# Kernel tuning notes

Hardware: AMD Instinct MI355X
Metric: run time of the kernel (lower is better)

## Reference

```python
import jax, jax.numpy as jnp
import numpy as np

B, N, D_FEAT = 4, 2048, 3
P = B * N
C_KP, K_PTS, NSAMPLE = 64, 15, 64
RADIUS, WINDOW = 0.2, 0.25
KP_EXTENT = 0.08  # prev_grid_size * sigma
F, H, HID, L = 256, 8, 512, 2
DH = F // H
EPS = 1e-5


def setup_inputs() -> dict:
    key = jax.random.key(0)
    k = jax.random.split(key, 24)
    s = 0.02
    position = jax.random.uniform(k[0], (B, N, 3), jnp.float32)
    feature = jax.random.normal(k[1], (B, N, D_FEAT), jnp.float32)
    # KPConv kernel points: fixed points inside a ball of radius 1.5*KP_EXTENT
    d = jax.random.normal(k[2], (K_PTS, 3))
    d = d / jnp.clip(jnp.linalg.norm(d, axis=1, keepdims=True), 1e-6)
    r = jax.random.uniform(k[3], (K_PTS, 1)) ** (1.0 / 3.0)
    kernel_points = (d * r * 1.5 * KP_EXTENT).astype(jnp.float32)
    return dict(
        position=position,
        feature=feature,
        kernel_points=kernel_points,
        kp_weights=s * jax.random.normal(k[4], (K_PTS, D_FEAT, C_KP), jnp.float32),
        bn_gamma=jnp.ones((C_KP,), jnp.float32),
        bn_beta=jnp.zeros((C_KP,), jnp.float32),
        weightmatrix=jax.random.normal(k[5], (1, C_KP + 3, F), jnp.float32) * s,
        Wq=s * jax.random.normal(k[6], (L, F, F), jnp.float32),
        bq=jnp.zeros((L, F), jnp.float32),
        Wk=s * jax.random.normal(k[7], (L, F, F), jnp.float32),
        bk=jnp.zeros((L, F), jnp.float32),
        Wv=s * jax.random.normal(k[8], (L, F, F), jnp.float32),
        bv=jnp.zeros((L, F), jnp.float32),
        Wo=s * jax.random.normal(k[9], (L, F, F), jnp.float32),
        bo=jnp.zeros((L, F), jnp.float32),
        ln1_g=jnp.ones((L, F), jnp.float32),
        ln1_b=jnp.zeros((L, F), jnp.float32),
        W1=s * jax.random.normal(k[10], (L, F, HID), jnp.float32),
        b1=jnp.zeros((L, HID), jnp.float32),
        W2=s * jax.random.normal(k[11], (L, HID, F), jnp.float32),
        b2=jnp.zeros((L, F), jnp.float32),
        ln2_g=jnp.ones((L, F), jnp.float32),
        ln2_b=jnp.zeros((L, F), jnp.float32),
    )


def _ball_query(position):
    """partial_dense ball query: first NSAMPLE in-radius neighbors per point, fill=P."""
    def one(b, pb):
        d2 = jnp.sum((pb[:, None, :] - pb[None, :, :]) ** 2, -1)      # [N,N]
        within = d2 <= RADIUS ** 2
        # stable argsort puts in-radius indices first, in ascending index order
        order = jnp.argsort(jnp.where(within, 0, 1).astype(jnp.int32), axis=1)[:, :NSAMPLE]
        valid = jnp.arange(NSAMPLE)[None, :] < jnp.sum(within, axis=1)[:, None]
        return jnp.where(valid, order + b * N, P)
    return jax.vmap(one)(jnp.arange(B), position).reshape(P, NSAMPLE)


def _kpconv(pos_flat, feat_flat, idx, kernel_points, kp_weights, bn_gamma, bn_beta):
    pos_pad = jnp.concatenate([pos_flat, jnp.full((1, 3), 1e6, pos_flat.dtype)], 0)
    feat_pad = jnp.concatenate([feat_flat, jnp.zeros((1, feat_flat.shape[1]), feat_flat.dtype)], 0)
    neigh = pos_pad[idx] - pos_flat[:, None, :]                     # [P,NS,3]
    diff = neigh[:, :, None, :] - kernel_points[None, None]         # [P,NS,K,3]
    dist = jnp.sqrt(jnp.sum(diff * diff, -1) + 1e-12)               # [P,NS,K]
    infl = jnp.clip(1.0 - dist / KP_EXTENT, 0.0)                    # linear influence
    nf = feat_pad[idx]                                              # [P,NS,Din]
    wf = jnp.einsum('pnk,pnd->pkd', infl, nf)
    out = jnp.einsum('pkd,kdc->pc', wf, kp_weights)                 # [P,C]
    mu = out.mean(0)
    var = out.var(0)
    out = bn_gamma * (out - mu) * jax.lax.rsqrt(var + EPS) + bn_beta
    return jnp.where(out >= 0, out, 0.2 * out)                      # LeakyReLU(0.2)


def _cluster_mask(position):
    """grid_sample: same-voxel points attend to each other. Returns bool [B,N,N]."""
    start = position.min(axis=1, keepdims=True)
    cell = jnp.floor((position - start) / WINDOW).astype(jnp.int32)
    cid = cell[..., 0] * 4096 + cell[..., 1] * 64 + cell[..., 2]
    return cid[:, :, None] == cid[:, None, :]


def _ln(x, g, b):
    mu = x.mean(-1, keepdims=True)
    v = x.var(-1, keepdims=True)
    return g * (x - mu) * jax.lax.rsqrt(v + EPS) + b


def _enc(x, mask, Wq, bq, Wk, bk, Wv, bv, Wo, bo, g1, be1, W1, bb1, W2, bb2, g2, be2):
    q = (x @ Wq + bq).reshape(B, N, H, DH)
    k = (x @ Wk + bk).reshape(B, N, H, DH)
    v = (x @ Wv + bv).reshape(B, N, H, DH)
    s = jnp.einsum('bihd,bjhd->bhij', q, k) * (1.0 / np.sqrt(DH))
    s = jnp.where(mask[:, None, :, :], s, -1e9)
    p = jax.nn.softmax(s, -1)
    o = jnp.einsum('bhij,bjhd->bihd', p, v).reshape(B, N, F)
    x = _ln(x + o @ Wo + bo, g1, be1)
    h = jax.nn.relu(x @ W1 + bb1) @ W2 + bb2
    return _ln(x + h, g2, be2)


def reference(position, feature, kernel_points, kp_weights, bn_gamma, bn_beta, weightmatrix,
              Wq, bq, Wk, bk, Wv, bv, Wo, bo, ln1_g, ln1_b, W1, b1, W2, b2, ln2_g, ln2_b):
    pos_flat = position.reshape(P, 3)
    feat_flat = feature.reshape(P, D_FEAT)
    idx = _ball_query(position)
    kpf = _kpconv(pos_flat, feat_flat, idx, kernel_points, kp_weights, bn_gamma, bn_beta)
    kpf = kpf.reshape(B, N, C_KP)
    mask = _cluster_mask(position)
    pw = jnp.concatenate([position, kpf], -1)                       # [B,N,C+3]
    emb = jnp.einsum('bnc,cf->bnf', pw, weightmatrix[0])
    for l in range(L):
        emb = _enc(emb, mask, Wq[l], bq[l], Wk[l], bk[l], Wv[l], bv[l], Wo[l], bo[l],
                   ln1_g[l], ln1_b[l], W1[l], b1[l], W2[l], b2[l], ln2_g[l], ln2_b[l])
    return emb
```

## Files before the change

kernel.cpp:

```cpp
#include <hip/hip_runtime.h>
#include <math.h>

#define BATCH 4
#define NPTS  2048
#define PTS   8192
#define NS    64
#define KPTS  15
#define CKP   64
#define FDIM  256
#define HIDD  512
#define NHEAD 8
#define DHEAD 32
#define NLAY  2
#define R2    0.04f
#define KPE   0.08f
#define WIN   0.25f
#define EPSF  1e-5f
#define SCALE 0.17677669529663687f
#define CPITCH 264

typedef __attribute__((ext_vector_type(8))) short          short8;
typedef __attribute__((ext_vector_type(8))) unsigned short ushort8;
typedef __attribute__((ext_vector_type(4))) float          f32x4;

static __device__ __forceinline__ unsigned short f2bf(float f) {
    unsigned int u = __float_as_uint(f);
    unsigned int r = u + 0x7fffu + ((u >> 16) & 1u);
    return (unsigned short)(r >> 16);
}
static __device__ __forceinline__ float b2f(unsigned short u) {
    return __uint_as_float(((unsigned int)u) << 16);
}

__global__ __launch_bounds__(256) void prep_k(
    const float* __restrict__ pos,
    const float* __restrict__ Wq, const float* __restrict__ Wk,
    const float* __restrict__ Wv, const float* __restrict__ Wo,
    const float* __restrict__ W1, const float* __restrict__ W2,
    const float* __restrict__ bq, const float* __restrict__ bk,
    const float* __restrict__ bv,
    unsigned short* __restrict__ wT, float* __restrict__ bqkv,
    int* __restrict__ sorted, int* __restrict__ inv,
    int* __restrict__ offs, int* __restrict__ hist,
    unsigned long long* __restrict__ masks)
{
    __shared__ __align__(16) unsigned char sm[38400];
    int bid = blockIdx.x, tid = threadIdx.x;

    if (bid < 3072) {
        int z = bid >> 8, r = bid & 255;
        int bx = r & 15, by = r >> 4;
        int t = z >> 1, l = z & 1;
        const float* src; unsigned short* dst; int K, N;
        switch (t) {
            case 0: src=Wq+(size_t)l*65536;  dst=wT+(size_t)l*196608;           K=256; N=256; break;
            case 1: src=Wk+(size_t)l*65536;  dst=wT+(size_t)l*196608+65536;     K=256; N=256; break;
            case 2: src=Wv+(size_t)l*65536;  dst=wT+(size_t)l*196608+131072;    K=256; N=256; break;
            case 3: src=Wo+(size_t)l*65536;  dst=wT+393216+(size_t)l*65536;     K=256; N=256; break;
            case 4: src=W1+(size_t)l*131072; dst=wT+524288+(size_t)l*131072;    K=256; N=512; break;
            default:src=W2+(size_t)l*131072; dst=wT+786432+(size_t)l*131072;    K=512; N=256; break;
        }
        int n0 = bx*32, k0 = by*32;
        if (n0 >= N || k0 >= K) return;
        float* ld = (float*)sm;
        #pragma unroll
        for (int i = 0; i < 4; ++i) { int v=tid+i*256; int ty=v>>5, tx=v&31;
            ld[ty*33+tx] = src[(size_t)(k0+ty)*N + n0+tx]; }
        __syncthreads();
        #pragma unroll
        for (int i = 0; i < 4; ++i) { int v=tid+i*256; int ny=v>>5, nk=v&31;
            dst[(size_t)(n0+ny)*K + k0+nk] = f2bf(ld[nk*33+ny]); }
    } else if (bid < 3584) {
        int m_ = bid - 3072;
        int chunk = m_ & 31, b = (m_ >> 5) & 3, qg = m_ >> 7;
        int w = tid >> 6, lane = tid & 63;
        float* qx = (float*)sm; float* qy = qx + 512; float* qz = qy + 512;
        int qbase = qg * 512;
        for (int t = tid; t < 512; t += 256) {
            const float* q = pos + (size_t)(b*NPTS + qbase + t)*3;
            qx[t] = q[0]; qy[t] = q[1]; qz[t] = q[2];
        }
        const float* c = pos + (size_t)(b*NPTS + chunk*64 + lane)*3;
        float cx = c[0], cy = c[1], cz = c[2];
        __syncthreads();
        int q0 = w * 128;
        for (int i = 0; i < 128; ++i) {
            int qi = q0 + i;
            float dx = cx - qx[qi], dy = cy - qy[qi], dz = cz - qz[qi];
            float d2 = dx*dx + dy*dy + dz*dz;
            unsigned long long m = __ballot(d2 <= R2);
            if (lane == 0) masks[(size_t)(b*NPTS + qbase + qi)*32 + chunk] = m;
        }
    } else if (bid < 3588) {
        int b = bid - 3584;
        float* sx = (float*)sm; float* sy = sx + 256; float* sz = sy + 256;
        unsigned char* cid_s = sm + 3072;
        unsigned int* maskc = (unsigned int*)(sm + 5120);
        int* wpfx = (int*)(sm + 21504);
        int* tot  = (int*)(sm + 37888);
        int* off_c= (int*)(sm + 38144);
        float mx=1e30f, my=1e30f, mz=1e30f;
        for (int n = tid; n < NPTS; n += 256) {
            const float* q = pos + ((size_t)b*NPTS + n)*3;
            mx = fminf(mx, q[0]); my = fminf(my, q[1]); mz = fminf(mz, q[2]);
        }
        sx[tid]=mx; sy[tid]=my; sz[tid]=mz; __syncthreads();
        for (int o=128;o;o>>=1){ if(tid<o){sx[tid]=fminf(sx[tid],sx[tid+o]);sy[tid]=fminf(sy[tid],sy[tid+o]);sz[tid]=fminf(sz[tid],sz[tid+o]);} __syncthreads(); }
        float X = sx[0], Y = sy[0], Z = sz[0];
        __syncthreads();
        for (int i = tid; i < 64*64; i += 256) maskc[i] = 0u;
        __syncthreads();
        for (int n = tid; n < NPTS; n += 256) {
            const float* q = pos + ((size_t)b*NPTS + n)*3;
            int cx = (int)floorf((q[0]-X)/WIN);
            int cy = (int)floorf((q[1]-Y)/WIN);
            int cz = (int)floorf((q[2]-Z)/WIN);
            int c = (cx<<4) | (cy<<2) | cz;
            cid_s[n] = (unsigned char)c;
            atomicOr(&maskc[c*64 + (n>>5)], 1u << (n & 31));
        }
        __syncthreads();
        if (tid < 64) {
            int run = 0;
            for (int wd = 0; wd < 64; ++wd) { wpfx[tid*64+wd] = run; run += __popc(maskc[tid*64+wd]); }
            tot[tid] = run;
        }
        __syncthreads();
        if (tid == 0) { int run = 0; for (int c = 0; c < 64; ++c) { off_c[c] = run; run += tot[c]; } }
        __syncthreads();
        if (tid < 64) { hist[b*64+tid] = tot[tid]; offs[b*64+tid] = off_c[tid]; }
        for (int n = tid; n < NPTS; n += 256) {
            int c = cid_s[n];
            int wd = n >> 5;
            int rank = wpfx[c*64+wd] + __popc(maskc[c*64+wd] & ((1u << (n & 31)) - 1u));
            int slot = b*NPTS + off_c[c] + rank;
            int p = b*NPTS + n;
            sorted[slot] = p;
            inv[p] = slot;
        }
    } else {
        int i = (bid - 3588)*256 + tid;
        if (i < 2*768) {
            int l = i / 768, n = i - l*768;
            float v = (n < 256) ? bq[l*256+n] : (n < 512) ? bk[l*256+n-256] : bv[l*256+n-512];
            bqkv[l*768 + n] = v;
        }
    }
}

__global__ __launch_bounds__(256) void kpc_k(
    const float* __restrict__ pos, const float* __restrict__ feat,
    const unsigned long long* __restrict__ masks,
    const float* __restrict__ kpts, const float* __restrict__ kpw,
    float* __restrict__ raw)
{
    __shared__ int   idxs[64][66];
    __shared__ float kpwl[45*64];
    __shared__ float kpl[48];
    __shared__ float wfp[64*181 + 4];

    int tid = threadIdx.x, w = tid >> 6, lane = tid & 63;
    int pb = blockIdx.x * 64;
    int b = pb >> 11;
    int base = b * NPTS;

    for (int t = tid; t < 45*64; t += 256) kpwl[t] = kpw[t];
    if (tid < 45) kpl[tid] = kpts[tid];

    int g = tid >> 5, j = tid & 31;
    for (int pp = 0; pp < 8; ++pp) {
        int lp = pp*8 + g;
        unsigned long long m = masks[(size_t)(pb + lp)*32 + j];
        int cnt = __popcll(m);
        int inc = cnt;
        #pragma unroll
        for (int off = 1; off < 32; off <<= 1) {
            int v = __shfl_up(inc, off, 32);
            if (j >= off) inc += v;
        }
        int pfx = inc - cnt;
        int total = __shfl(inc, 31, 32);
        unsigned long long mm = m; int slot = pfx;
        while (mm && slot < NS) {
            int bit = __ffsll((long long)mm) - 1;
            idxs[lp][slot++] = j*64 + bit;
            mm &= mm - 1;
        }
        int cc = total < NS ? total : NS;
        for (int s = cc + j; s < NS; s += 32) idxs[lp][s] = NPTS;
    }
    __syncthreads();

    float wf[45];
    #pragma unroll
    for (int t = 0; t < 45; ++t) wf[t] = 0.f;
    {
        int p = pb + lane;
        float xi = pos[(size_t)p*3+0], yi = pos[(size_t)p*3+1], zi = pos[(size_t)p*3+2];
        for (int n = w*16; n < w*16 + 16; ++n) {
            int id = idxs[lane][n];
            if (id < NPTS) {
                const float* pq = pos + (size_t)(base + id)*3;
                float rx = pq[0]-xi, ry = pq[1]-yi, rz = pq[2]-zi;
                const float* ff = feat + (size_t)(base + id)*3;
                float g0 = ff[0], g1 = ff[1], g2 = ff[2];
                #pragma unroll
                for (int k = 0; k < KPTS; ++k) {
                    float dx = rx - kpl[k*3+0], dy = ry - kpl[k*3+1], dz = rz - kpl[k*3+2];
                    float dist = sqrtf(dx*dx + dy*dy + dz*dz + 1e-12f);
                    float infl = fmaxf(0.f, 1.0f - dist * (1.0f/KPE));
                    wf[k*3+0] = fmaf(infl, g0, wf[k*3+0]);
                    wf[k*3+1] = fmaf(infl, g1, wf[k*3+1]);
                    wf[k*3+2] = fmaf(infl, g2, wf[k*3+2]);
                }
            }
        }
    }
    #pragma unroll
    for (int t = 0; t < 45; ++t) wfp[lane*181 + t*4 + w] = wf[t];
    __syncthreads();
    for (int i = tid; i < 64*45; i += 256) {
        int p_ = i / 45, t = i - p_*45;
        float* q = &wfp[p_*181 + t*4];
        q[0] = (q[0]+q[1]) + (q[2]+q[3]);
    }
    __syncthreads();
    {
        int c = tid & 63, pg = tid >> 6;
        float kw[45];
        #pragma unroll
        for (int t = 0; t < 45; ++t) kw[t] = kpwl[t*64 + c];
        for (int p0 = 0; p0 < 16; p0 += 4) {
            float a0=0.f, a1=0.f, a2=0.f, a3=0.f;
            int pl = pg*16 + p0;
            #pragma unroll
            for (int t = 0; t < 45; ++t) {
                a0 = fmaf(kw[t], wfp[(pl+0)*181 + t*4], a0);
                a1 = fmaf(kw[t], wfp[(pl+1)*181 + t*4], a1);
                a2 = fmaf(kw[t], wfp[(pl+2)*181 + t*4], a2);
                a3 = fmaf(kw[t], wfp[(pl+3)*181 + t*4], a3);
            }
            raw[(size_t)(pb + pl+0)*CKP + c] = a0;
            raw[(size_t)(pb + pl+1)*CKP + c] = a1;
            raw[(size_t)(pb + pl+2)*CKP + c] = a2;
            raw[(size_t)(pb + pl+3)*CKP + c] = a3;
        }
    }
}

__global__ void bn_stats_k(const float* __restrict__ raw, float* __restrict__ stats)
{
    int c = blockIdx.x, tid = threadIdx.x;
    float s = 0.f, q = 0.f;
    for (int p = tid; p < PTS; p += 256) { float v = raw[p*CKP + c]; s += v; q += v*v; }
    __shared__ float sh[256], sh2[256];
    sh[tid]=s; sh2[tid]=q; __syncthreads();
    for (int o = 128; o; o >>= 1) { if (tid < o) { sh[tid]+=sh[tid+o]; sh2[tid]+=sh2[tid+o]; } __syncthreads(); }
    if (tid == 0) { stats[c] = sh[0]; stats[CKP + c] = sh2[0]; }
}

__global__ void embed_k(const float* __restrict__ pos, const float* __restrict__ raw,
                        const float* __restrict__ stats, const float* __restrict__ gamma,
                        const float* __restrict__ beta, const float* __restrict__ Wm,
                        const int* __restrict__ inv,
                        float* __restrict__ xs, unsigned short* __restrict__ xsb)
{
    int p = blockIdx.x, tid = threadIdx.x;
    __shared__ float pw[67];
    if (tid < 3) pw[tid] = pos[p*3 + tid];
    else if (tid < 67) {
        int c = tid - 3;
        float mu  = stats[c] * (1.0f/PTS);
        float var = stats[CKP+c] * (1.0f/PTS) - mu*mu;
        float v = raw[p*CKP + c];
        float h = gamma[c] * (v - mu) * rsqrtf(var + EPSF) + beta[c];
        pw[tid] = h >= 0.f ? h : 0.2f * h;
    }
    __syncthreads();
    float acc = 0.f;
    for (int c = 0; c < 67; ++c) acc += pw[c] * Wm[c*FDIM + tid];
    int slot = inv[p];
    xs[(size_t)slot*FDIM + tid] = acc;
    xsb[(size_t)slot*FDIM + tid] = f2bf(acc);
}

template<int ACT, int LNM>
__global__ __launch_bounds__(256) void bgemm256_k(
    const unsigned short* __restrict__ A, const unsigned short* __restrict__ Wt,
    const float* __restrict__ bias, const float* __restrict__ R,
    const float* __restrict__ g, const float* __restrict__ be,
    const int* __restrict__ sorted,
    float* __restrict__ Cf, unsigned short* __restrict__ Cb,
    int Nc, int K)
{
    __shared__ unsigned short As[32*72];
    __shared__ unsigned short Bs[256*72];
    __shared__ float red_s[4][32], red_q[4][32];
    int tid = threadIdx.x;
    int l = tid & 63, wc = tid >> 6;
    int lr = l & 15, lk = l >> 4;
    int bm = blockIdx.y * 32, bn = blockIdx.x * 256;

    f32x4 acc[2][4] = {};

    for (int k0 = 0; k0 < K; k0 += 64) {
        __syncthreads();
        {
            int row = tid >> 3, seg = tid & 7;
            *(ushort8*)&As[row*72 + seg*8] =
                *(const ushort8*)&A[(size_t)(bm + row)*K + k0 + seg*8];
        }
        #pragma unroll
        for (int i = 0; i < 8; ++i) {
            int id = tid + i*256;
            int row = id >> 3, seg = id & 7;
            *(ushort8*)&Bs[row*72 + seg*8] =
                *(const ushort8*)&Wt[(size_t)(bn + row)*K + k0 + seg*8];
        }
        __syncthreads();
        #pragma unroll
        for (int kk = 0; kk < 64; kk += 32) {
            short8 a[2], b[4];
            #pragma unroll
            for (int mi = 0; mi < 2; ++mi)
                a[mi] = *(const short8*)&As[(mi*16 + lr)*72 + kk + lk*8];
            #pragma unroll
            for (int ni = 0; ni < 4; ++ni)
                b[ni] = *(const short8*)&Bs[(wc*64 + ni*16 + lr)*72 + kk + lk*8];
            #pragma unroll
            for (int mi = 0; mi < 2; ++mi)
                #pragma unroll
                for (int ni = 0; ni < 4; ++ni)
                    acc[mi][ni] = __builtin_amdgcn_mfma_f32_16x16x32_bf16(
                        a[mi], b[ni], acc[mi][ni], 0, 0, 0);
        }
    }

    #pragma unroll
    for (int mi = 0; mi < 2; ++mi) {
        #pragma unroll
        for (int r = 0; r < 4; ++r) {
            int row = bm + mi*16 + lk*4 + r;
            #pragma unroll
            for (int ni = 0; ni < 4; ++ni) {
                int col = bn + wc*64 + ni*16 + lr;
                float v = acc[mi][ni][r] + bias[col];
                if (R) v += R[(size_t)row*Nc + col];
                if (ACT == 1) v = v > 0.f ? v : 0.f;
                acc[mi][ni][r] = v;
            }
        }
    }

    if (LNM == 0) {
        #pragma unroll
        for (int mi = 0; mi < 2; ++mi)
            #pragma unroll
            for (int r = 0; r < 4; ++r) {
                int row = bm + mi*16 + lk*4 + r;
                #pragma unroll
                for (int ni = 0; ni < 4; ++ni) {
                    int col = bn + wc*64 + ni*16 + lr;
                    if (Cf) Cf[(size_t)row*Nc + col] = acc[mi][ni][r];
                    if (Cb) Cb[(size_t)row*Nc + col] = f2bf(acc[mi][ni][r]);
                }
            }
    } else {
        #pragma unroll
        for (int mi = 0; mi < 2; ++mi) {
            #pragma unroll
            for (int r = 0; r < 4; ++r) {
                float ps = 0.f, pq = 0.f;
                #pragma unroll
                for (int ni = 0; ni < 4; ++ni) { float v = acc[mi][ni][r]; ps += v; pq += v*v; }
                ps += __shfl_xor(ps, 1);  pq += __shfl_xor(pq, 1);
                ps += __shfl_xor(ps, 2);  pq += __shfl_xor(pq, 2);
                ps += __shfl_xor(ps, 4);  pq += __shfl_xor(pq, 4);
                ps += __shfl_xor(ps, 8);  pq += __shfl_xor(pq, 8);
                if (lr == 0) {
                    int rl = mi*16 + lk*4 + r;
                    red_s[wc][rl] = ps;
                    red_q[wc][rl] = pq;
                }
            }
        }
        __syncthreads();
        #pragma unroll
        for (int mi = 0; mi < 2; ++mi) {
            #pragma unroll
            for (int r = 0; r < 4; ++r) {
                int rl = mi*16 + lk*4 + r;
                float s = red_s[0][rl] + red_s[1][rl] + red_s[2][rl] + red_s[3][rl];
                float q = red_q[0][rl] + red_q[1][rl] + red_q[2][rl] + red_q[3][rl];
                float mu  = s * (1.0f/FDIM);
                float var = q * (1.0f/FDIM) - mu*mu;
                float rs  = rsqrtf(var + EPSF);
                int row = bm + rl;
                #pragma unroll
                for (int ni = 0; ni < 4; ++ni) {
                    int col = wc*64 + ni*16 + lr;
                    float o = g[col]*(acc[mi][ni][r]-mu)*rs + be[col];
                    if (LNM == 2) Cf[(size_t)sorted[row]*FDIM + col] = o;
                    else          Cf[(size_t)row*FDIM + col] = o;
                    if (Cb) Cb[(size_t)row*FDIM + col] = f2bf(o);
                }
            }
        }
    }
}

__global__ __launch_bounds__(512) void attn_k(
    const unsigned short* __restrict__ qkv, const int* __restrict__ offs,
    const int* __restrict__ hist, unsigned short* __restrict__ o)
{
    int cci = blockIdx.x, b = blockIdx.y;
    int Mc = hist[b*64 + cci];
    if (Mc == 0) return;
    int off = b*NPTS + offs[b*64 + cci];
    __shared__ unsigned short Kl[64*CPITCH];
    __shared__ unsigned short Vl[64*CPITCH];
    __shared__ unsigned short Pl[8][64*72];
    int tid = threadIdx.x;

    if (Mc <= 64) {
        #pragma unroll
        for (int it = 0; it < 4; ++it) {
            int id = tid + it*512;
            int key = id >> 5, ch8 = (id & 31)*8;
            ushort8 kv, vv;
            if (key < Mc) {
                kv = *(const ushort8*)&qkv[(size_t)(off+key)*768 + 256 + ch8];
                vv = *(const ushort8*)&qkv[(size_t)(off+key)*768 + 512 + ch8];
            } else {
                kv = (ushort8)0; vv = (ushort8)0;
            }
            *(ushort8*)&Kl[key*CPITCH + ch8] = kv;
            *(ushort8*)&Vl[key*CPITCH + ch8] = vv;
        }
        __syncthreads();

        int w = tid >> 6, l = tid & 63;
        int h = w;
        int lr = l & 15, lk = l >> 4;

        f32x4 s[4][4] = {};
        short8 a[4], bb[4];
        #pragma unroll
        for (int mi = 0; mi < 4; ++mi) {
            int rg = off + mi*16 + lr;
            if (rg > PTS-1) rg = PTS-1;
            a[mi] = *(const short8*)&qkv[(size_t)rg*768 + h*32 + lk*8];
        }
        #pragma unroll
        for (int ni = 0; ni < 4; ++ni)
            bb[ni] = *(const short8*)&Kl[(ni*16+lr)*CPITCH + h*32 + lk*8];
        #pragma unroll
        for (int mi = 0; mi < 4; ++mi)
            #pragma unroll
            for (int ni = 0; ni < 4; ++ni)
                s[mi][ni] = __builtin_amdgcn_mfma_f32_16x16x32_bf16(a[mi], bb[ni], s[mi][ni], 0, 0, 0);

        unsigned short* Pw = Pl[w];
        float invl[4][4];
        #pragma unroll
        for (int mi = 0; mi < 4; ++mi) {
            #pragma unroll
            for (int r = 0; r < 4; ++r) {
                int row = mi*16 + lk*4 + r;
                float sv[4]; float mx = -1e30f;
                #pragma unroll
                for (int ni = 0; ni < 4; ++ni) {
                    int col = ni*16 + lr;
                    float x = s[mi][ni][r] * SCALE;
                    sv[ni] = (col < Mc) ? x : -1e30f;
                    mx = fmaxf(mx, sv[ni]);
                }
                mx = fmaxf(mx, __shfl_xor(mx, 1));
                mx = fmaxf(mx, __shfl_xor(mx, 2));
                mx = fmaxf(mx, __shfl_xor(mx, 4));
                mx = fmaxf(mx, __shfl_xor(mx, 8));
                float ls = 0.f;
                #pragma unroll
                for (int ni = 0; ni < 4; ++ni) {
                    float e = __expf(sv[ni] - mx);
                    ls += e;
                    Pw[row*72 + ni*16 + lr] = f2bf(e);
                }
                ls += __shfl_xor(ls, 1);
                ls += __shfl_xor(ls, 2);
                ls += __shfl_xor(ls, 4);
                ls += __shfl_xor(ls, 8);
                invl[mi][r] = 1.0f / ls;
            }
        }

        f32x4 oacc[4][2] = {};
        #pragma unroll
        for (int ks = 0; ks < 2; ++ks) {
            short8 bv[2];
            #pragma unroll
            for (int db = 0; db < 2; ++db) {
                short8 t;
                #pragma unroll
                for (int e = 0; e < 8; ++e)
                    t[e] = (short)Vl[(ks*32 + lk*8 + e)*CPITCH + h*32 + db*16 + lr];
                bv[db] = t;
            }
            #pragma unroll
            for (int mi = 0; mi < 4; ++mi) {
                short8 pa = *(const short8*)&Pw[(mi*16+lr)*72 + ks*32 + lk*8];
                #pragma unroll
                for (int db = 0; db < 2; ++db)
                    oacc[mi][db] = __builtin_amdgcn_mfma_f32_16x16x32_bf16(pa, bv[db], oacc[mi][db], 0, 0, 0);
            }
        }

        #pragma unroll
        for (int mi = 0; mi < 4; ++mi)
            #pragma unroll
            for (int db = 0; db < 2; ++db)
                #pragma unroll
                for (int r = 0; r < 4; ++r) {
                    int row = mi*16 + lk*4 + r;
                    if (row < Mc)
                        o[(size_t)(off+row)*FDIM + h*32 + db*16 + lr] =
                            f2bf(oacc[mi][db][r] * invl[mi][r]);
                }
    } else {
        for (int task = tid; task < Mc*NHEAD; task += 512) {
            int row = task >> 3, h = task & 7;
            float qr[DHEAD];
            #pragma unroll
            for (int d = 0; d < DHEAD; ++d)
                qr[d] = b2f(qkv[(size_t)(off+row)*768 + h*32 + d]);
            float m = -3e38f, lsum = 0.f, acc[DHEAD];
            #pragma unroll
            for (int d = 0; d < DHEAD; ++d) acc[d] = 0.f;
            for (int j = 0; j < Mc; ++j) {
                float dot = 0.f;
                #pragma unroll
                for (int d = 0; d < DHEAD; ++d)
                    dot += qr[d] * b2f(qkv[(size_t)(off+j)*768 + 256 + h*32 + d]);
                float sc = dot * SCALE;
                float mn = fmaxf(m, sc);
                float aa = __expf(m - mn);
                float e  = __expf(sc - mn);
                lsum = lsum*aa + e;
                #pragma unroll
                for (int d = 0; d < DHEAD; ++d)
                    acc[d] = acc[d]*aa + e * b2f(qkv[(size_t)(off+j)*768 + 512 + h*32 + d]);
                m = mn;
            }
            float inv = 1.0f / lsum;
            #pragma unroll
            for (int d = 0; d < DHEAD; ++d)
                o[(size_t)(off+row)*FDIM + h*32 + d] = f2bf(acc[d]*inv);
        }
    }
}

extern "C" void kernel_launch(void* const* d_in, const int* in_sizes, int n_in,
                              void* d_out, int out_size, void* d_ws, size_t ws_size,
                              hipStream_t stream)
{
    (void)in_sizes; (void)n_in; (void)out_size; (void)ws_size;
    const float* pos  = (const float*)d_in[0];
    const float* feat = (const float*)d_in[1];
    const float* kpts = (const float*)d_in[2];
    const float* kpw  = (const float*)d_in[3];
    const float* bn_g = (const float*)d_in[4];
    const float* bn_b = (const float*)d_in[5];
    const float* Wm   = (const float*)d_in[6];
    const float* Wq   = (const float*)d_in[7];
    const float* bq   = (const float*)d_in[8];
    const float* Wk   = (const float*)d_in[9];
    const float* bk   = (const float*)d_in[10];
    const float* Wv   = (const float*)d_in[11];
    const float* bv   = (const float*)d_in[12];
    const float* Wo   = (const float*)d_in[13];
    const float* bo   = (const float*)d_in[14];
    const float* g1   = (const float*)d_in[15];
    const float* be1  = (const float*)d_in[16];
    const float* W1   = (const float*)d_in[17];
    const float* bb1  = (const float*)d_in[18];
    const float* W2   = (const float*)d_in[19];
    const float* bb2  = (const float*)d_in[20];
    const float* g2   = (const float*)d_in[21];
    const float* be2  = (const float*)d_in[22];

    char* ws = (char*)d_ws;
    const size_t MB = 1024*1024;
    float* raw    = (float*)(ws + 0);
    unsigned long long* masks = (unsigned long long*)(ws + 2*MB);
    float* stats  = (float*)(ws + 4*MB);
    int*   hist   = (int*)(ws + 4*MB + 4096);
    int*   offs   = hist + 256;
    int*   sorted = (int*)(ws + 4*MB + 16384);
    int*   inv    = sorted + PTS;
    float* xs   = (float*)(ws + 5*MB);
    float* x2   = (float*)(ws + 13*MB);
    unsigned short* xsb   = (unsigned short*)(ws + 21*MB);
    unsigned short* x2b   = (unsigned short*)(ws + 25*MB);
    unsigned short* qkvb  = (unsigned short*)(ws + 29*MB);
    unsigned short* attnb = (unsigned short*)(ws + 41*MB);
    unsigned short* wT    = (unsigned short*)(ws + 45*MB);
    float*          bqkv  = (float*)(ws + 47*MB);
    unsigned short* hb    = qkvb;

    prep_k<<<3594, 256, 0, stream>>>(pos, Wq, Wk, Wv, Wo, W1, W2, bq, bk, bv,
                                     wT, bqkv, sorted, inv, offs, hist, masks);
    kpc_k<<<PTS/64, 256, 0, stream>>>(pos, feat, masks, kpts, kpw, raw);
    bn_stats_k<<<CKP, 256, 0, stream>>>(raw, stats);
    embed_k<<<PTS, 256, 0, stream>>>(pos, raw, stats, bn_g, bn_b, Wm, inv, xs, xsb);

    for (int l = 0; l < NLAY; ++l) {
        bgemm256_k<0,0><<<dim3(3, PTS/32), 256, 0, stream>>>(
            xsb, wT + (size_t)l*196608, bqkv + l*768, nullptr, nullptr, nullptr, nullptr,
            nullptr, qkvb, 768, FDIM);
        attn_k<<<dim3(64, BATCH), 512, 0, stream>>>(qkvb, offs, hist, attnb);
        bgemm256_k<0,1><<<dim3(1, PTS/32), 256, 0, stream>>>(
            attnb, wT + 393216 + (size_t)l*65536, bo + l*FDIM, xs,
            g1 + l*FDIM, be1 + l*FDIM, nullptr, x2, x2b, FDIM, FDIM);
        bgemm256_k<1,0><<<dim3(2, PTS/32), 256, 0, stream>>>(
            x2b, wT + 524288 + (size_t)l*131072, bb1 + l*HIDD, nullptr, nullptr, nullptr,
            nullptr, nullptr, hb, HIDD, FDIM);
        if (l == NLAY-1)
            bgemm256_k<0,2><<<dim3(1, PTS/32), 256, 0, stream>>>(
                hb, wT + 786432 + (size_t)l*131072, bb2 + l*FDIM, x2,
                g2 + l*FDIM, be2 + l*FDIM, sorted, (float*)d_out, nullptr, FDIM, HIDD);
        else
            bgemm256_k<0,1><<<dim3(1, PTS/32), 256, 0, stream>>>(
                hb, wT + 786432 + (size_t)l*131072, bb2 + l*FDIM, x2,
                g2 + l*FDIM, be2 + l*FDIM, nullptr, xs, xsb, FDIM, HIDD);
    }
}
```

Before: 239.1 us.

## Fuse FFN up and down GEMMs into one kernel; enlarge QKV GEMM row tile

Adds an ffn_k kernel that computes the ReLU hidden activation in 64-wide chunks into shared memory and immediately accumulates the second projection, then applies residual and LayerNorm. This removes the hidden-activation round trip through global memory and one kernel launch per layer. The QKV GEMM is also templated to take 64 rows per block instead of 32, halving its grid. The fused kernel uses roughly 90KB of shared memory and reloads both weight matrices per 32-row block, which may limit occupancy.

Result: faster. 224.3 us (-6.2%).

```diff
diff --git a/kernel.cpp b/kernel.cpp
--- a/kernel.cpp
+++ b/kernel.cpp
@@ -284,7 +284,7 @@
     xsb[(size_t)slot*FDIM + tid] = f2bf(acc);
 }
 
-template<int ACT, int LNM>
+template<int ACT, int LNM, int MR>
 __global__ __launch_bounds__(256) void bgemm256_k(
     const unsigned short* __restrict__ A, const unsigned short* __restrict__ Wt,
     const float* __restrict__ bias, const float* __restrict__ R,
@@ -293,20 +293,22 @@
     float* __restrict__ Cf, unsigned short* __restrict__ Cb,
     int Nc, int K)
 {
-    __shared__ unsigned short As[32*72];
+    __shared__ unsigned short As[MR*16*72];
     __shared__ unsigned short Bs[256*72];
     __shared__ float red_s[4][32], red_q[4][32];
     int tid = threadIdx.x;
     int l = tid & 63, wc = tid >> 6;
     int lr = l & 15, lk = l >> 4;
-    int bm = blockIdx.y * 32, bn = blockIdx.x * 256;
-
-    f32x4 acc[2][4] = {};
+    int bm = blockIdx.y * (MR*16), bn = blockIdx.x * 256;
+
+    f32x4 acc[MR][4] = {};
 
     for (int k0 = 0; k0 < K; k0 += 64) {
         __syncthreads();
-        {
-            int row = tid >> 3, seg = tid & 7;
+        #pragma unroll
+        for (int i = 0; i < MR/2; ++i) {
+            int id = tid + i*256;
+            int row = id >> 3, seg = id & 7;
             *(ushort8*)&As[row*72 + seg*8] =
                 *(const ushort8*)&A[(size_t)(bm + row)*K + k0 + seg*8];
         }
@@ -320,15 +322,15 @@
         __syncthreads();
         #pragma unroll
         for (int kk = 0; kk < 64; kk += 32) {
-            short8 a[2], b[4];
-            #pragma unroll
-            for (int mi = 0; mi < 2; ++mi)
+            short8 a[MR], b[4];
+            #pragma unroll
+            for (int mi = 0; mi < MR; ++mi)
                 a[mi] = *(const short8*)&As[(mi*16 + lr)*72 + kk + lk*8];
             #pragma unroll
             for (int ni = 0; ni < 4; ++ni)
                 b[ni] = *(const short8*)&Bs[(wc*64 + ni*16 + lr)*72 + kk + lk*8];
             #pragma unroll
-            for (int mi = 0; mi < 2; ++mi)
+            for (int mi = 0; mi < MR; ++mi)
                 #pragma unroll
                 for (int ni = 0; ni < 4; ++ni)
                     acc[mi][ni] = __builtin_amdgcn_mfma_f32_16x16x32_bf16(
@@ -337,7 +339,7 @@
     }
 
     #pragma unroll
-    for (int mi = 0; mi < 2; ++mi) {
+    for (int mi = 0; mi < MR; ++mi) {
         #pragma unroll
         for (int r = 0; r < 4; ++r) {
             int row = bm + mi*16 + lk*4 + r;
@@ -354,7 +356,7 @@
 
     if (LNM == 0) {
         #pragma unroll
-        for (int mi = 0; mi < 2; ++mi)
+        for (int mi = 0; mi < MR; ++mi)
             #pragma unroll
             for (int r = 0; r < 4; ++r) {
                 int row = bm + mi*16 + lk*4 + r;
@@ -404,6 +406,151 @@
                     else          Cf[(size_t)row*FDIM + col] = o;
                     if (Cb) Cb[(size_t)row*FDIM + col] = f2bf(o);
                 }
+            }
+        }
+    }
+}
+
+template<int FINAL>
+__global__ __launch_bounds__(256) void ffn_k(
+    const unsigned short* __restrict__ A,
+    const unsigned short* __restrict__ W1T,
+    const float* __restrict__ b1,
+    const unsigned short* __restrict__ W2T,
+    const float* __restrict__ b2,
+    const float* __restrict__ R,
+    const float* __restrict__ g, const float* __restrict__ be,
+    const int* __restrict__ sorted,
+    float* __restrict__ Cf, unsigned short* __restrict__ Cb)
+{
+    __shared__ unsigned short As[32*264];
+    __shared__ unsigned short Bs1[64*264];
+    __shared__ unsigned short Bs2[256*72];
+    __shared__ unsigned short Hs[32*72];
+    __shared__ float red_s[4][32], red_q[4][32];
+
+    int tid = threadIdx.x;
+    int l = tid & 63, wc = tid >> 6;
+    int lr = l & 15, lk = l >> 4;
+    int bm = blockIdx.x * 32;
+
+    #pragma unroll
+    for (int i = 0; i < 4; ++i) {
+        int id = tid + i*256;
+        int row = id >> 5, seg = id & 31;
+        *(ushort8*)&As[row*264 + seg*8] =
+            *(const ushort8*)&A[(size_t)(bm + row)*FDIM + seg*8];
+    }
+
+    f32x4 acc[2][4] = {};
+
+    for (int hc = 0; hc < 8; ++hc) {
+        __syncthreads();
+        #pragma unroll
+        for (int i = 0; i < 8; ++i) {
+            int id = tid + i*256;
+            int row = id >> 5, seg = id & 31;
+            *(ushort8*)&Bs1[row*264 + seg*8] =
+                *(const ushort8*)&W1T[(size_t)(hc*64 + row)*FDIM + seg*8];
+        }
+        #pragma unroll
+        for (int i = 0; i < 8; ++i) {
+            int id = tid + i*256;
+            int row = id >> 3, seg = id & 7;
+            *(ushort8*)&Bs2[row*72 + seg*8] =
+                *(const ushort8*)&W2T[(size_t)row*HIDD + hc*64 + seg*8];
+        }
+        __syncthreads();
+
+        f32x4 h[2] = {};
+        #pragma unroll
+        for (int kk = 0; kk < 256; kk += 32) {
+            short8 bfr = *(const short8*)&Bs1[(wc*16 + lr)*264 + kk + lk*8];
+            #pragma unroll
+            for (int mi = 0; mi < 2; ++mi) {
+                short8 a = *(const short8*)&As[(mi*16 + lr)*264 + kk + lk*8];
+                h[mi] = __builtin_amdgcn_mfma_f32_16x16x32_bf16(a, bfr, h[mi], 0, 0, 0);
+            }
+        }
+        #pragma unroll
+        for (int mi = 0; mi < 2; ++mi)
+            #pragma unroll
+            for (int r = 0; r < 4; ++r) {
+                int row = mi*16 + lk*4 + r;
+                int hcol = wc*16 + lr;
+                float v = h[mi][r] + b1[hc*64 + hcol];
+                v = v > 0.f ? v : 0.f;
+                Hs[row*72 + hcol] = f2bf(v);
+            }
+        __syncthreads();
+
+        #pragma unroll
+        for (int kk = 0; kk < 64; kk += 32) {
+            short8 pa[2], wb[4];
+            #pragma unroll
+            for (int mi = 0; mi < 2; ++mi)
+                pa[mi] = *(const short8*)&Hs[(mi*16 + lr)*72 + kk + lk*8];
+            #pragma unroll
+            for (int ni = 0; ni < 4; ++ni)
+                wb[ni] = *(const short8*)&Bs2[(wc*64 + ni*16 + lr)*72 + kk + lk*8];
+            #pragma unroll
+            for (int mi = 0; mi < 2; ++mi)
+                #pragma unroll
+                for (int ni = 0; ni < 4; ++ni)
+                    acc[mi][ni] = __builtin_amdgcn_mfma_f32_16x16x32_bf16(
+                        pa[mi], wb[ni], acc[mi][ni], 0, 0, 0);
+        }
+    }
+
+    #pragma unroll
+    for (int mi = 0; mi < 2; ++mi) {
+        #pragma unroll
+        for (int r = 0; r < 4; ++r) {
+            int row = bm + mi*16 + lk*4 + r;
+            #pragma unroll
+            for (int ni = 0; ni < 4; ++ni) {
+                int col = wc*64 + ni*16 + lr;
+                acc[mi][ni][r] += b2[col] + R[(size_t)row*FDIM + col];
+            }
+        }
+    }
+    #pragma unroll
+    for (int mi = 0; mi < 2; ++mi) {
+        #pragma unroll
+        for (int r = 0; r < 4; ++r) {
+            float ps = 0.f, pq = 0.f;
+            #pragma unroll
+            for (int ni = 0; ni < 4; ++ni) { float v = acc[mi][ni][r]; ps += v; pq += v*v; }
+            ps += __shfl_xor(ps, 1);  pq += __shfl_xor(pq, 1);
+            ps += __shfl_xor(ps, 2);  pq += __shfl_xor(pq, 2);
+            ps += __shfl_xor(ps, 4);  pq += __shfl_xor(pq, 4);
+            ps += __shfl_xor(ps, 8);  pq += __shfl_xor(pq, 8);
+            if (lr == 0) {
+                int rl = mi*16 + lk*4 + r;
+                red_s[wc][rl] = ps;
+                red_q[wc][rl] = pq;
+            }
+        }
+    }
+    __syncthreads();
+    #pragma unroll
+    for (int mi = 0; mi < 2; ++mi) {
+        #pragma unroll
+        for (int r = 0; r < 4; ++r) {
+            int rl = mi*16 + lk*4 + r;
+            float s = red_s[0][rl] + red_s[1][rl] + red_s[2][rl] + red_s[3][rl];
+            float q = red_q[0][rl] + red_q[1][rl] + red_q[2][rl] + red_q[3][rl];
+            float mu  = s * (1.0f/FDIM);
+            float var = q * (1.0f/FDIM) - mu*mu;
+            float rs  = rsqrtf(var + EPSF);
+            int row = bm + rl;
+            #pragma unroll
+            for (int ni = 0; ni < 4; ++ni) {
+                int col = wc*64 + ni*16 + lr;
+                float o = g[col]*(acc[mi][ni][r]-mu)*rs + be[col];
+                if (FINAL) Cf[(size_t)sorted[row]*FDIM + col] = o;
+                else       Cf[(size_t)row*FDIM + col] = o;
+                if (Cb) Cb[(size_t)row*FDIM + col] = f2bf(o);
             }
         }
     }
@@ -605,7 +752,6 @@
     unsigned short* attnb = (unsigned short*)(ws + 41*MB);
     unsigned short* wT    = (unsigned short*)(ws + 45*MB);
     float*          bqkv  = (float*)(ws + 47*MB);
-    unsigned short* hb    = qkvb;
 
     prep_k<<<3594, 256, 0, stream>>>(pos, Wq, Wk, Wv, Wo, W1, W2, bq, bk, bv,
                                      wT, bqkv, sorted, inv, offs, hist, masks);
@@ -614,23 +760,22 @@
     embed_k<<<PTS, 256, 0, stream>>>(pos, raw, stats, bn_g, bn_b, Wm, inv, xs, xsb);
 
     for (int l = 0; l < NLAY; ++l) {
-        bgemm256_k<0,0><<<dim3(3, PTS/32), 256, 0, stream>>>(
+        const unsigned short* W1T_l = wT + 524288 + (size_t)l*131072;
+        const unsigned short* W2T_l = wT + 786432 + (size_t)l*131072;
+        bgemm256_k<0,0,4><<<dim3(3, PTS/64), 256, 0, stream>>>(
             xsb, wT + (size_t)l*196608, bqkv + l*768, nullptr, nullptr, nullptr, nullptr,
             nullptr, qkvb, 768, FDIM);
         attn_k<<<dim3(64, BATCH), 512, 0, stream>>>(qkvb, offs, hist, attnb);
-        bgemm256_k<0,1><<<dim3(1, PTS/32), 256, 0, stream>>>(
+        bgemm256_k<0,1,2><<<dim3(1, PTS/32), 256, 0, stream>>>(
             attnb, wT + 393216 + (size_t)l*65536, bo + l*FDIM, xs,
             g1 + l*FDIM, be1 + l*FDIM, nullptr, x2, x2b, FDIM, FDIM);
-        bgemm256_k<1,0><<<dim3(2, PTS/32), 256, 0, stream>>>(
-            x2b, wT + 524288 + (size_t)l*131072, bb1 + l*HIDD, nullptr, nullptr, nullptr,
-            nullptr, nullptr, hb, HIDD, FDIM);
         if (l == NLAY-1)
-            bgemm256_k<0,2><<<dim3(1, PTS/32), 256, 0, stream>>>(
-                hb, wT + 786432 + (size_t)l*131072, bb2 + l*FDIM, x2,
-                g2 + l*FDIM, be2 + l*FDIM, sorted, (float*)d_out, nullptr, FDIM, HIDD);
+            ffn_k<1><<<PTS/32, 256, 0, stream>>>(
+                x2b, W1T_l, bb1 + l*HIDD, W2T_l, bb2 + l*FDIM, x2,
+                g2 + l*FDIM, be2 + l*FDIM, sorted, (float*)d_out, nullptr);
         else
-            bgemm256_k<0,1><<<dim3(1, PTS/32), 256, 0, stream>>>(
-                hb, wT + 786432 + (size_t)l*131072, bb2 + l*FDIM, x2,
-                g2 + l*FDIM, be2 + l*FDIM, nullptr, xs, xsb, FDIM, HIDD);
-    }
-}
+            ffn_k<0><<<PTS/32, 256, 0, stream>>>(
+                x2b, W1T_l, bb1 + l*HIDD, W2T_l, bb2 + l*FDIM, x2,
+                g2 + l*FDIM, be2 + l*FDIM, nullptr, xs, xsb);
+    }
+}
```
